# Kernel tuning notes

Measured on AMD Instinct MI355X. Metric: run time of the kernel, lower is better.

Reference implementation:

```python
import jax, jax.numpy as jnp
import numpy as np

N, E, D, H, DH = 10000, 160000, 1024, 4, 256  # nodes, edges, feat dim, heads, per-head dim
NB, G = 3, 64  # num_blocks, num graphs in batch
NEG_SLOPE = 0.2  # PyG GATConv default


def setup_inputs() -> dict:
    key = jax.random.key(0)
    ks = jax.random.split(key, 8)
    x = jax.random.normal(ks[0], (N, D), jnp.float32)
    edge_index = jax.random.randint(ks[1], (2, E), 0, N)
    batch = jnp.sort(jax.random.randint(ks[2], (N,), 0, G))
    W = jax.random.normal(ks[3], (NB, D, H * DH), jnp.float32) * 0.03
    a_src = jax.random.normal(ks[4], (NB, H, DH), jnp.float32) * 0.1
    a_dst = jax.random.normal(ks[5], (NB, H, DH), jnp.float32) * 0.1
    b = jnp.zeros((NB, H * DH), jnp.float32)
    Wr = jax.random.normal(ks[6], (D, 2), jnp.float32) * 0.03
    br = jnp.zeros((2,), jnp.float32)
    return dict(x=x, edge_index=edge_index, batch=batch, W=W, a_src=a_src,
                a_dst=a_dst, b=b, Wr=Wr, br=br)


def _gat_conv(x, src, dst, W, asrc, adst, bias):
    # Linear projection per head: [N, H, DH]
    h = (x @ W).reshape(N, H, DH)
    # Per-node attention logits (src/dst halves of the GAT attention vector)
    es = jnp.einsum('nhd,hd->nh', h, asrc)  # [N, H]
    ed = jnp.einsum('nhd,hd->nh', h, adst)  # [N, H]
    # Edge scores + LeakyReLU
    e = jax.nn.leaky_relu(es[src] + ed[dst], NEG_SLOPE)  # [Etot, H]
    # Segment softmax over edges sharing the same destination node
    m = jax.ops.segment_max(e, dst, num_segments=N)
    p = jnp.exp(e - m[dst])
    s = jax.ops.segment_sum(p, dst, num_segments=N)
    alpha = p / (s[dst] + 1e-16)  # [Etot, H]
    # Scatter-aggregate weighted source features
    out = jax.ops.segment_sum(h[src] * alpha[:, :, None], dst, num_segments=N)
    return out.reshape(N, H * DH) + bias


def reference(x, edge_index, batch, W, a_src, a_dst, b, Wr, br):
    # PyG GATConv adds self-loops by default
    loops = jnp.arange(N)
    src = jnp.concatenate([edge_index[0], loops])
    dst = jnp.concatenate([edge_index[1], loops])
    # Faithful to the source: each block reads the ORIGINAL x; dropout in eval mode.
    h = x
    for i in range(NB):
        h = jax.nn.relu(_gat_conv(x, src, dst, W[i], a_src[i], a_dst[i], b[i]))
    # global_mean_pool over graph assignment `batch`
    sums = jax.ops.segment_sum(h, batch, num_segments=G)
    cnt = jax.ops.segment_sum(jnp.ones((N, 1), h.dtype), batch, num_segments=G)
    pooled = sums / jnp.maximum(cnt, 1.0)
    return pooled @ Wr + br
```

## Files before the change

kernel.cpp:

```cpp
#include <hip/hip_runtime.h>
#include <hip/hip_bf16.h>

#define N_NODES 10000
#define N_EDGES 160000
#define ETOT    (N_NODES + N_EDGES)
#define DIM     1024
#define NHEAD   4
#define DHEAD   256
#define NGRAPH  64
#define NEG_SLOPE 0.2f

typedef short  bf16x8 __attribute__((ext_vector_type(8)));
typedef float  f32x4  __attribute__((ext_vector_type(4)));
typedef unsigned short u16x4 __attribute__((ext_vector_type(4)));
typedef unsigned short u16x8 __attribute__((ext_vector_type(8)));

__device__ __forceinline__ unsigned short f2bf_rne(float v) {
    unsigned u = __builtin_bit_cast(unsigned, v);
    return (unsigned short)((u + 0x7fffu + ((u >> 16) & 1u)) >> 16);
}
__device__ __forceinline__ float bf2f(unsigned short b) {
    return __builtin_bit_cast(float, (unsigned)b << 16);
}
__device__ __forceinline__ float lrelu(float x) { return x > 0.f ? x : NEG_SLOPE * x; }


__global__ __launch_bounds__(256) void prep_x(const float* __restrict__ x,
                                              unsigned short* __restrict__ xhi,
                                              unsigned short* __restrict__ xlo) {
    int i = blockIdx.x * 256 + threadIdx.x;
    if (i >= N_NODES * 128) return;
    int row = i >> 7, kseg = i & 127;
    const float* src = x + (size_t)row * DIM + kseg * 8;
    f32x4 v0 = *(const f32x4*)src;
    f32x4 v1 = *(const f32x4*)(src + 4);
    u16x8 hi, lo;
#pragma unroll
    for (int j = 0; j < 4; ++j) {
        unsigned short hb = f2bf_rne(v0[j]);
        hi[j] = hb; lo[j] = f2bf_rne(v0[j] - bf2f(hb));
    }
#pragma unroll
    for (int j = 0; j < 4; ++j) {
        unsigned short hb = f2bf_rne(v1[j]);
        hi[4 + j] = hb; lo[4 + j] = f2bf_rne(v1[j] - bf2f(hb));
    }
    size_t off = (size_t)(row >> 4) * 16384 + (kseg >> 2) * 512 + (kseg & 3) * 128 + (row & 15) * 8;
    *(u16x8*)(xhi + off) = hi;
    *(u16x8*)(xlo + off) = lo;
}

__global__ __launch_bounds__(256) void prep_w(const float* __restrict__ W2,
                                              unsigned short* __restrict__ wthi,
                                              unsigned short* __restrict__ wtlo,
                                              float* __restrict__ es,
                                              float* __restrict__ ed,
                                              int* __restrict__ cnt,
                                              int* __restrict__ curs,
                                              int* __restrict__ gcnt,
                                              int* __restrict__ gbeg,
                                              int* __restrict__ gend) {
    __shared__ float tile[64][65];
    int bc = blockIdx.x;
    int bk = blockIdx.y;
    int t = threadIdx.x;

    int gid = (blockIdx.y * gridDim.x + blockIdx.x) * 256 + t;
    if (gid < NGRAPH) { gcnt[gid] = 0; gbeg[gid] = 0x7fffffff; gend[gid] = -1; }
    if (gid < N_NODES) { cnt[gid] = 1; curs[gid] = 0; }
    if (gid < N_NODES * 4) { es[gid] = 0.f; ed[gid] = 0.f; }

    int tj = t & 63, ti = t >> 6;
#pragma unroll
    for (int u = 0; u < 16; ++u) {
        int r = u * 4 + ti;
        tile[r][tj] = W2[(size_t)(bk * 64 + r) * DIM + bc * 64 + tj];
    }
    __syncthreads();
#pragma unroll
    for (int u = 0; u < 16; ++u) {
        int cr = u * 4 + ti;
        float v = tile[tj][cr];
        unsigned short hb = f2bf_rne(v);
        float rres = v - bf2f(hb);
        int col = bc * 64 + cr;
        int k = bk * 64 + tj;
        size_t o = (size_t)(col >> 4) * 16384 + (k >> 5) * 512
                 + ((k >> 3) & 3) * 128 + (col & 15) * 8 + (k & 7);
        wthi[o] = hb;
        wtlo[o] = f2bf_rne(rres);
    }
}

#define BM 128
#define BN 128
#define BK 32
#define NROWT ((N_NODES + BM - 1) / BM)
#define NCOLT (DIM / BN)

__global__ __launch_bounds__(256) void gemm3(const unsigned short* __restrict__ xhi,
                                             const unsigned short* __restrict__ xlo,
                                             const unsigned short* __restrict__ wthi,
                                             const unsigned short* __restrict__ wtlo,
                                             const float* __restrict__ asrc,
                                             const float* __restrict__ adst,
                                             unsigned short* __restrict__ hb,
                                             float* __restrict__ es,
                                             float* __restrict__ ed) {
    const int id = blockIdx.x;
    const int xcd = id & 7;
    const int br = xcd + 8 * (id >> 6);
    const int bc = (id >> 3) & 7;
    if (br >= NROWT) return;
    const int r0 = br * BM;
    const int c0 = bc * BN;

    __shared__ short lds[4][BM * BK];
    const int t = threadIdx.x;
    const int lane = t & 63, wid = t >> 6;
    const int wm = wid >> 1, wn = wid & 1;

    const unsigned short* const srcs[4] = {xhi, xlo, wthi, wtlo};
    const int g0 = ((wid < 2) ? r0 : c0) >> 4;
    const unsigned short* gsrc = srcs[wid] + (size_t)g0 * 16384 + (size_t)lane * 8;

    f32x4 acc[4][4];
#pragma unroll
    for (int mi = 0; mi < 4; ++mi)
#pragma unroll
        for (int ni = 0; ni < 4; ++ni) acc[mi][ni] = (f32x4){0.f, 0.f, 0.f, 0.f};

    for (int kt = 0; kt < DIM / BK; ++kt) {
        __syncthreads();
#pragma unroll
        for (int j = 0; j < 8; ++j) {
            const unsigned short* g = gsrc + (size_t)j * 16384 + (size_t)kt * 512;
            __builtin_amdgcn_global_load_lds(
                (const __attribute__((address_space(1))) unsigned int*)g,
                (__attribute__((address_space(3))) unsigned int*)&lds[wid][j * 512],
                16, 0, 0);
        }
        __syncthreads();

        bf16x8 ahi[4], alo[4], bhi[4], blo[4];
#pragma unroll
        for (int mi = 0; mi < 4; ++mi) {
            int sub = wm * 4 + mi;
            ahi[mi] = *(const bf16x8*)&lds[0][sub * 512 + lane * 8];
            alo[mi] = *(const bf16x8*)&lds[1][sub * 512 + lane * 8];
        }
#pragma unroll
        for (int ni = 0; ni < 4; ++ni) {
            int sub = wn * 4 + ni;
            bhi[ni] = *(const bf16x8*)&lds[2][sub * 512 + lane * 8];
            blo[ni] = *(const bf16x8*)&lds[3][sub * 512 + lane * 8];
        }
#pragma unroll
        for (int mi = 0; mi < 4; ++mi)
#pragma unroll
            for (int ni = 0; ni < 4; ++ni) {
                f32x4 c = acc[mi][ni];
                c = __builtin_amdgcn_mfma_f32_16x16x32_bf16(ahi[mi], bhi[ni], c, 0, 0, 0);
                c = __builtin_amdgcn_mfma_f32_16x16x32_bf16(ahi[mi], blo[ni], c, 0, 0, 0);
                c = __builtin_amdgcn_mfma_f32_16x16x32_bf16(alo[mi], bhi[ni], c, 0, 0, 0);
                acc[mi][ni] = c;
            }
    }

#pragma unroll
    for (int mi = 0; mi < 4; ++mi)
#pragma unroll
        for (int ni = 0; ni < 4; ++ni)
#pragma unroll
            for (int v = 0; v < 4; ++v) {
                int row = r0 + wm * 64 + mi * 16 + ((lane >> 4) << 2) + v;
                if (row < N_NODES) {
                    int col = c0 + wn * 64 + ni * 16 + (lane & 15);
                    hb[(size_t)row * DIM + col] = f2bf_rne(acc[mi][ni][v]);
                }
            }

    const int head = c0 >> 8;
    float as_c[4], ad_c[4];
#pragma unroll
    for (int ni = 0; ni < 4; ++ni) {
        int col = c0 + wn * 64 + ni * 16 + (lane & 15);
        as_c[ni] = asrc[col];
        ad_c[ni] = adst[col];
    }
#pragma unroll
    for (int mi = 0; mi < 4; ++mi)
#pragma unroll
        for (int v = 0; v < 4; ++v) {
            float pe = 0.f, pd = 0.f;
#pragma unroll
            for (int ni = 0; ni < 4; ++ni) {
                float a = acc[mi][ni][v];
                pe += a * as_c[ni];
                pd += a * ad_c[ni];
            }
#pragma unroll
            for (int d = 1; d < 16; d <<= 1) {
                pe += __shfl_xor(pe, d);
                pd += __shfl_xor(pd, d);
            }
            int row = r0 + wm * 64 + mi * 16 + ((lane >> 4) << 2) + v;
            if ((lane & 15) == 0 && row < N_NODES) {
                atomicAdd(es + row * 4 + head, pe);
                atomicAdd(ed + row * 4 + head, pd);
            }
        }
}

__global__ void graph_k(const int* __restrict__ dst, const int* __restrict__ batch,
                        int* cnt, int* gcnt, int* gbeg, int* gend) {
    int e = blockIdx.x * 256 + threadIdx.x;
    if (e < N_EDGES) atomicAdd(cnt + dst[e], 1);
    if (e < N_NODES) {
        int b = batch[e];
        atomicAdd(gcnt + b, 1);
        atomicMin(gbeg + b, e);
        atomicMax(gend + b, e);
    }
}

__global__ __launch_bounds__(1024) void scan_k(const int* __restrict__ cnt, int* __restrict__ off) {
    __shared__ int wsh[16];
    __shared__ int tot_s;
    int t = threadIdx.x, lane = t & 63, wv = t >> 6;
    int running = 0;
    for (int c0 = 0; c0 < N_NODES; c0 += 1024) {
        int i = c0 + t;
        int v = (i < N_NODES) ? cnt[i] : 0;
        int s = v;
#pragma unroll
        for (int d = 1; d < 64; d <<= 1) {
            int y = __shfl_up(s, d);
            if (lane >= d) s += y;
        }
        if (lane == 63) wsh[wv] = s;
        __syncthreads();
        if (wv == 0) {
            int wsv = (lane < 16) ? wsh[lane] : 0;
            int e = wsv;
#pragma unroll
            for (int d = 1; d < 16; d <<= 1) {
                int y = __shfl_up(e, d);
                if (lane >= d) e += y;
            }
            if (lane < 16) wsh[lane] = e - wsv;
            if (lane == 15) tot_s = e;
        }
        __syncthreads();
        if (i < N_NODES) off[i] = running + wsh[wv] + s - v;
        running += tot_s;
    }
}

__global__ void bucket_k(const int* __restrict__ src, const int* __restrict__ dst,
                         const int* __restrict__ off, int* cursor, int* bucket) {
    int e = blockIdx.x * 256 + threadIdx.x;
    if (e >= ETOT) return;
    int d = (e < N_EDGES) ? dst[e] : (e - N_EDGES);
    int pos = atomicAdd(cursor + d, 1);
    bucket[off[d] + pos] = e;
}

#define HCAP 192
__global__ __launch_bounds__(256) void aggregate_k(const unsigned short* __restrict__ hb,
                                                   const float* __restrict__ es,
                                                   const float* __restrict__ ed,
                                                   const int* __restrict__ src,
                                                   const int* __restrict__ cnt,
                                                   const int* __restrict__ off,
                                                   const int* __restrict__ bucket,
                                                   const float* __restrict__ b2,
                                                   float* __restrict__ out) {
    int n = blockIdx.x, t = threadIdx.x;
    int deg = cnt[n], base = off[n];
    f32x4 edn = *(const f32x4*)(ed + (size_t)n * 4);
    __shared__ int  s_src[HCAP];
    __shared__ f32x4 s_e[HCAP];
    __shared__ f32x4 wred[4];

    f32x4 m4 = {-3e38f, -3e38f, -3e38f, -3e38f};
    for (int i = t; i < deg; i += 256) {
        int eid = bucket[base + i];
        int s = (eid < N_EDGES) ? src[eid] : (eid - N_EDGES);
        f32x4 e4 = *(const f32x4*)(es + (size_t)s * 4);
        e4.x = lrelu(e4.x + edn.x); e4.y = lrelu(e4.y + edn.y);
        e4.z = lrelu(e4.z + edn.z); e4.w = lrelu(e4.w + edn.w);
        if (i < HCAP) { s_src[i] = s; s_e[i] = e4; }
        m4.x = fmaxf(m4.x, e4.x); m4.y = fmaxf(m4.y, e4.y);
        m4.z = fmaxf(m4.z, e4.z); m4.w = fmaxf(m4.w, e4.w);
    }
#pragma unroll
    for (int d = 1; d < 64; d <<= 1) {
        m4.x = fmaxf(m4.x, __shfl_xor(m4.x, d));
        m4.y = fmaxf(m4.y, __shfl_xor(m4.y, d));
        m4.z = fmaxf(m4.z, __shfl_xor(m4.z, d));
        m4.w = fmaxf(m4.w, __shfl_xor(m4.w, d));
    }
    if ((t & 63) == 0) wred[t >> 6] = m4;
    __syncthreads();
    f32x4 mm = wred[0];
#pragma unroll
    for (int w = 1; w < 4; ++w) {
        mm.x = fmaxf(mm.x, wred[w].x); mm.y = fmaxf(mm.y, wred[w].y);
        mm.z = fmaxf(mm.z, wred[w].z); mm.w = fmaxf(mm.w, wred[w].w);
    }
    int hd = t >> 6;
    float mh = hd == 0 ? mm.x : hd == 1 ? mm.y : hd == 2 ? mm.z : mm.w;

    f32x4 acc = {0.f, 0.f, 0.f, 0.f};
    float sump = 0.f;
    for (int i = 0; i < deg; ++i) {
        int s;
        f32x4 e4;
        if (i < HCAP) { s = s_src[i]; e4 = s_e[i]; }
        else {
            int eid = bucket[base + i];
            s = (eid < N_EDGES) ? src[eid] : (eid - N_EDGES);
            e4 = *(const f32x4*)(es + (size_t)s * 4);
            e4.x = lrelu(e4.x + edn.x); e4.y = lrelu(e4.y + edn.y);
            e4.z = lrelu(e4.z + edn.z); e4.w = lrelu(e4.w + edn.w);
        }
        float eh = hd == 0 ? e4.x : hd == 1 ? e4.y : hd == 2 ? e4.z : e4.w;
        float p = expf(eh - mh);
        sump += p;
        u16x4 q = *(const u16x4*)(hb + (size_t)s * DIM + t * 4);
        f32x4 hv = {bf2f(q[0]), bf2f(q[1]), bf2f(q[2]), bf2f(q[3])};
        acc += p * hv;
    }
    float inv = 1.0f / (sump + 1e-16f);
    f32x4 bb = *(const f32x4*)(b2 + t * 4);
    f32x4 r = acc * inv + bb;
    r.x = fmaxf(r.x, 0.f); r.y = fmaxf(r.y, 0.f);
    r.z = fmaxf(r.z, 0.f); r.w = fmaxf(r.w, 0.f);
    *(f32x4*)(out + (size_t)n * DIM + t * 4) = r;
}

__global__ __launch_bounds__(256) void pool_k(const float* __restrict__ out,
                                              const int* __restrict__ gbeg,
                                              const int* __restrict__ gend,
                                              float* __restrict__ pooled) {
    int g = blockIdx.x, c = blockIdx.y, t = threadIdx.x;
    int col = c * 256 + t;
    int b0 = gbeg[g], b1 = gend[g];
    float acc = 0.f;
    for (int n = b0; n <= b1; ++n) acc += out[(size_t)n * DIM + col];
    pooled[(size_t)g * DIM + col] = acc;
}

__global__ __launch_bounds__(256) void final_k(const float* __restrict__ pooled,
                                               const int* __restrict__ gcnt,
                                               const float* __restrict__ Wr,
                                               const float* __restrict__ br,
                                               float* __restrict__ out) {
    int g = blockIdx.x, t = threadIdx.x;
    float s0 = 0.f, s1 = 0.f;
    for (int d = t; d < DIM; d += 256) {
        float v = pooled[(size_t)g * DIM + d];
        s0 += v * Wr[d * 2];
        s1 += v * Wr[d * 2 + 1];
    }
    __shared__ float r0[256], r1[256];
    r0[t] = s0; r1[t] = s1;
    __syncthreads();
    for (int st = 128; st > 0; st >>= 1) {
        if (t < st) { r0[t] += r0[t + st]; r1[t] += r1[t + st]; }
        __syncthreads();
    }
    if (t == 0) {
        float c = fmaxf((float)gcnt[g], 1.f);
        out[g * 2 + 0] = r0[0] / c + br[0];
        out[g * 2 + 1] = r1[0] / c + br[1];
    }
}

extern "C" void kernel_launch(void* const* d_in, const int* in_sizes, int n_in,
                              void* d_out, int out_size, void* d_ws, size_t ws_size,
                              hipStream_t stream) {
    (void)in_sizes; (void)n_in; (void)out_size; (void)ws_size;
    const float* x     = (const float*)d_in[0];
    const int*   ei    = (const int*)d_in[1];
    const int*   batch = (const int*)d_in[2];
    const float* W     = (const float*)d_in[3];
    const float* a_src = (const float*)d_in[4];
    const float* a_dst = (const float*)d_in[5];
    const float* b     = (const float*)d_in[6];
    const float* Wr    = (const float*)d_in[7];
    const float* br    = (const float*)d_in[8];

    const float* W2    = W + (size_t)2 * DIM * DIM;
    const float* asrc2 = a_src + 2 * NHEAD * DHEAD;
    const float* adst2 = a_dst + 2 * NHEAD * DHEAD;
    const float* b2    = b + 2 * DIM;
    const int* srcI = ei;
    const int* dstI = ei + N_EDGES;

    char* wsp = (char*)d_ws;
    size_t o = 0;
    auto alloc = [&](size_t bytes) -> char* {
        char* p = wsp + o;
        o = (o + bytes + 255) & ~(size_t)255;
        return p;
    };
    unsigned short* xhi  = (unsigned short*)alloc((size_t)N_NODES * DIM * 2);
    unsigned short* xlo  = (unsigned short*)alloc((size_t)N_NODES * DIM * 2);
    unsigned short* wthi = (unsigned short*)alloc((size_t)DIM * DIM * 2);
    unsigned short* wtlo = (unsigned short*)alloc((size_t)DIM * DIM * 2);
    unsigned short* hb   = (unsigned short*)alloc((size_t)N_NODES * DIM * 2);
    float* es   = (float*)alloc((size_t)N_NODES * 4 * 4);
    float* ed   = (float*)alloc((size_t)N_NODES * 4 * 4);
    int*   cnt  = (int*)alloc((size_t)N_NODES * 4);
    int*   offs = (int*)alloc((size_t)N_NODES * 4);
    int*   curs = (int*)alloc((size_t)N_NODES * 4);
    int*   bkt  = (int*)alloc((size_t)ETOT * 4);
    float* pooled = (float*)alloc((size_t)NGRAPH * DIM * 4);
    int*   gcnt   = (int*)alloc(NGRAPH * 4);
    int*   gbeg   = (int*)alloc(NGRAPH * 4);
    int*   gend   = (int*)alloc(NGRAPH * 4);
    float* outn = (float*)xhi;

    prep_x<<<(N_NODES * 128 + 255) / 256, 256, 0, stream>>>(x, xhi, xlo);
    prep_w<<<dim3(16, 16), 256, 0, stream>>>(W2, wthi, wtlo, es, ed, cnt, curs, gcnt, gbeg, gend);
    gemm3<<<((NROWT + 7) / 8) * 8 * NCOLT, 256, 0, stream>>>(xhi, xlo, wthi, wtlo,
                                                             asrc2, adst2, hb, es, ed);
    graph_k<<<(N_EDGES + 255) / 256, 256, 0, stream>>>(dstI, batch, cnt, gcnt, gbeg, gend);
    scan_k<<<1, 1024, 0, stream>>>(cnt, offs);
    bucket_k<<<(ETOT + 255) / 256, 256, 0, stream>>>(srcI, dstI, offs, curs, bkt);

    aggregate_k<<<N_NODES, 256, 0, stream>>>(hb, es, ed, srcI, cnt, offs, bkt, b2, outn);
    pool_k<<<dim3(NGRAPH, 4), 256, 0, stream>>>(outn, gbeg, gend, pooled);
    final_k<<<NGRAPH, 256, 0, stream>>>(pooled, gcnt, Wr, br, (float*)d_out);
}
```

Baseline: 422.8 us.

## Use row-major bf16 split layout, fuse prep with graph stats and pooling

Drops the pre-tiled 16-row MFMA layout for x and W. Both are now stored row-major as bf16 hi/lo, and the GEMM loads them with strided global_load_lds over a plain 2D grid, without the XCD-aware block swizzle. The x split conversion is merged with the edge/graph counting kernel into one launch, and mean-pooling is fused with the final linear head. The goal is fewer launches and no pooled buffer, at the cost of less coalesced global loads, possible LDS bank conflicts in the GEMM, and a pooling stage with fewer blocks.

```diff
diff --git a/kernel.cpp b/kernel.cpp
--- a/kernel.cpp
+++ b/kernel.cpp
@@ -24,31 +24,6 @@
 }
 __device__ __forceinline__ float lrelu(float x) { return x > 0.f ? x : NEG_SLOPE * x; }
 
-
-__global__ __launch_bounds__(256) void prep_x(const float* __restrict__ x,
-                                              unsigned short* __restrict__ xhi,
-                                              unsigned short* __restrict__ xlo) {
-    int i = blockIdx.x * 256 + threadIdx.x;
-    if (i >= N_NODES * 128) return;
-    int row = i >> 7, kseg = i & 127;
-    const float* src = x + (size_t)row * DIM + kseg * 8;
-    f32x4 v0 = *(const f32x4*)src;
-    f32x4 v1 = *(const f32x4*)(src + 4);
-    u16x8 hi, lo;
-#pragma unroll
-    for (int j = 0; j < 4; ++j) {
-        unsigned short hb = f2bf_rne(v0[j]);
-        hi[j] = hb; lo[j] = f2bf_rne(v0[j] - bf2f(hb));
-    }
-#pragma unroll
-    for (int j = 0; j < 4; ++j) {
-        unsigned short hb = f2bf_rne(v1[j]);
-        hi[4 + j] = hb; lo[4 + j] = f2bf_rne(v1[j] - bf2f(hb));
-    }
-    size_t off = (size_t)(row >> 4) * 16384 + (kseg >> 2) * 512 + (kseg & 3) * 128 + (row & 15) * 8;
-    *(u16x8*)(xhi + off) = hi;
-    *(u16x8*)(xlo + off) = lo;
-}
 
 __global__ __launch_bounds__(256) void prep_w(const float* __restrict__ W2,
                                               unsigned short* __restrict__ wthi,
@@ -83,12 +58,45 @@
         float v = tile[tj][cr];
         unsigned short hb = f2bf_rne(v);
         float rres = v - bf2f(hb);
-        int col = bc * 64 + cr;
-        int k = bk * 64 + tj;
-        size_t o = (size_t)(col >> 4) * 16384 + (k >> 5) * 512
-                 + ((k >> 3) & 3) * 128 + (col & 15) * 8 + (k & 7);
+        size_t o = (size_t)(bc * 64 + cr) * DIM + bk * 64 + tj;
         wthi[o] = hb;
         wtlo[o] = f2bf_rne(rres);
+    }
+}
+
+#define XBLK (N_NODES * DIM / 4 / 256)
+__global__ __launch_bounds__(256) void prep_xg(const float* __restrict__ x,
+                                               unsigned short* __restrict__ xhi,
+                                               unsigned short* __restrict__ xlo,
+                                               const int* __restrict__ dst,
+                                               const int* __restrict__ batch,
+                                               int* __restrict__ cnt,
+                                               int* __restrict__ gcnt,
+                                               int* __restrict__ gbeg,
+                                               int* __restrict__ gend) {
+    int bid = blockIdx.x;
+    if (bid < XBLK) {
+        int i = bid * 256 + threadIdx.x;
+        f32x4 v = *(const f32x4*)(x + (size_t)i * 4);
+        u16x4 hi, lo;
+#pragma unroll
+        for (int j = 0; j < 4; ++j) {
+            unsigned short hb = f2bf_rne(v[j]);
+            float r = v[j] - bf2f(hb);
+            hi[j] = hb;
+            lo[j] = f2bf_rne(r);
+        }
+        *(u16x4*)(xhi + (size_t)i * 4) = hi;
+        *(u16x4*)(xlo + (size_t)i * 4) = lo;
+    } else {
+        int e = (bid - XBLK) * 256 + threadIdx.x;
+        if (e < N_EDGES) atomicAdd(cnt + dst[e], 1);
+        if (e < N_NODES) {
+            int b = batch[e];
+            atomicAdd(gcnt + b, 1);
+            atomicMin(gbeg + b, e);
+            atomicMax(gend + b, e);
+        }
     }
 }
 
@@ -107,13 +115,8 @@
                                              unsigned short* __restrict__ hb,
                                              float* __restrict__ es,
                                              float* __restrict__ ed) {
-    const int id = blockIdx.x;
-    const int xcd = id & 7;
-    const int br = xcd + 8 * (id >> 6);
-    const int bc = (id >> 3) & 7;
-    if (br >= NROWT) return;
-    const int r0 = br * BM;
-    const int c0 = bc * BN;
+    const int r0 = blockIdx.y * BM;
+    const int c0 = blockIdx.x * BN;
 
     __shared__ short lds[4][BM * BK];
     const int t = threadIdx.x;
@@ -121,8 +124,8 @@
     const int wm = wid >> 1, wn = wid & 1;
 
     const unsigned short* const srcs[4] = {xhi, xlo, wthi, wtlo};
-    const int g0 = ((wid < 2) ? r0 : c0) >> 4;
-    const unsigned short* gsrc = srcs[wid] + (size_t)g0 * 16384 + (size_t)lane * 8;
+    const unsigned short* wbase = srcs[wid];
+    const int rowb = (wid < 2) ? r0 : c0;
 
     f32x4 acc[4][4];
 #pragma unroll
@@ -130,11 +133,15 @@
 #pragma unroll
         for (int ni = 0; ni < 4; ++ni) acc[mi][ni] = (f32x4){0.f, 0.f, 0.f, 0.f};
 
-    for (int kt = 0; kt < DIM / BK; ++kt) {
+    const int rL = lane & 15;
+    const int koff = (lane >> 4) * 8;
+
+    for (int k0 = 0; k0 < DIM; k0 += BK) {
         __syncthreads();
 #pragma unroll
         for (int j = 0; j < 8; ++j) {
-            const unsigned short* g = gsrc + (size_t)j * 16384 + (size_t)kt * 512;
+            const unsigned short* g = wbase
+                + (size_t)(rowb + j * 16 + (lane >> 2)) * DIM + k0 + (lane & 3) * 8;
             __builtin_amdgcn_global_load_lds(
                 (const __attribute__((address_space(1))) unsigned int*)g,
                 (__attribute__((address_space(3))) unsigned int*)&lds[wid][j * 512],
@@ -145,15 +152,15 @@
         bf16x8 ahi[4], alo[4], bhi[4], blo[4];
 #pragma unroll
         for (int mi = 0; mi < 4; ++mi) {
-            int sub = wm * 4 + mi;
-            ahi[mi] = *(const bf16x8*)&lds[0][sub * 512 + lane * 8];
-            alo[mi] = *(const bf16x8*)&lds[1][sub * 512 + lane * 8];
+            int row = wm * 64 + mi * 16 + rL;
+            ahi[mi] = *(const bf16x8*)&lds[0][row * BK + koff];
+            alo[mi] = *(const bf16x8*)&lds[1][row * BK + koff];
         }
 #pragma unroll
         for (int ni = 0; ni < 4; ++ni) {
-            int sub = wn * 4 + ni;
-            bhi[ni] = *(const bf16x8*)&lds[2][sub * 512 + lane * 8];
-            blo[ni] = *(const bf16x8*)&lds[3][sub * 512 + lane * 8];
+            int row = wn * 64 + ni * 16 + rL;
+            bhi[ni] = *(const bf16x8*)&lds[2][row * BK + koff];
+            blo[ni] = *(const bf16x8*)&lds[3][row * BK + koff];
         }
 #pragma unroll
         for (int mi = 0; mi < 4; ++mi)
@@ -210,18 +217,6 @@
                 atomicAdd(ed + row * 4 + head, pd);
             }
         }
-}
-
-__global__ void graph_k(const int* __restrict__ dst, const int* __restrict__ batch,
-                        int* cnt, int* gcnt, int* gbeg, int* gend) {
-    int e = blockIdx.x * 256 + threadIdx.x;
-    if (e < N_EDGES) atomicAdd(cnt + dst[e], 1);
-    if (e < N_NODES) {
-        int b = batch[e];
-        atomicAdd(gcnt + b, 1);
-        atomicMin(gbeg + b, e);
-        atomicMax(gend + b, e);
-    }
 }
 
 __global__ __launch_bounds__(1024) void scan_k(const int* __restrict__ cnt, int* __restrict__ off) {
@@ -340,41 +335,34 @@
     *(f32x4*)(out + (size_t)n * DIM + t * 4) = r;
 }
 
-__global__ __launch_bounds__(256) void pool_k(const float* __restrict__ out,
-                                              const int* __restrict__ gbeg,
-                                              const int* __restrict__ gend,
-                                              float* __restrict__ pooled) {
-    int g = blockIdx.x, c = blockIdx.y, t = threadIdx.x;
-    int col = c * 256 + t;
+__global__ __launch_bounds__(256) void poolfinal_k(const float* __restrict__ outn,
+                                                   const int* __restrict__ gcnt,
+                                                   const int* __restrict__ gbeg,
+                                                   const int* __restrict__ gend,
+                                                   const float* __restrict__ Wr,
+                                                   const float* __restrict__ br,
+                                                   float* __restrict__ out) {
+    int g = blockIdx.x, t = threadIdx.x;
     int b0 = gbeg[g], b1 = gend[g];
-    float acc = 0.f;
-    for (int n = b0; n <= b1; ++n) acc += out[(size_t)n * DIM + col];
-    pooled[(size_t)g * DIM + col] = acc;
-}
-
-__global__ __launch_bounds__(256) void final_k(const float* __restrict__ pooled,
-                                               const int* __restrict__ gcnt,
-                                               const float* __restrict__ Wr,
-                                               const float* __restrict__ br,
-                                               float* __restrict__ out) {
-    int g = blockIdx.x, t = threadIdx.x;
-    float s0 = 0.f, s1 = 0.f;
-    for (int d = t; d < DIM; d += 256) {
-        float v = pooled[(size_t)g * DIM + d];
-        s0 += v * Wr[d * 2];
-        s1 += v * Wr[d * 2 + 1];
-    }
-    __shared__ float r0[256], r1[256];
-    r0[t] = s0; r1[t] = s1;
+    f32x4 acc = {0.f, 0.f, 0.f, 0.f};
+    for (int n = b0; n <= b1; ++n)
+        acc += *(const f32x4*)(outn + (size_t)n * DIM + t * 4);
+    int c4 = t * 4;
+    float s0 = acc.x * Wr[c4 * 2]     + acc.y * Wr[(c4 + 1) * 2]
+             + acc.z * Wr[(c4 + 2) * 2] + acc.w * Wr[(c4 + 3) * 2];
+    float s1 = acc.x * Wr[c4 * 2 + 1]     + acc.y * Wr[(c4 + 1) * 2 + 1]
+             + acc.z * Wr[(c4 + 2) * 2 + 1] + acc.w * Wr[(c4 + 3) * 2 + 1];
+    __shared__ float r0s[256], r1s[256];
+    r0s[t] = s0; r1s[t] = s1;
     __syncthreads();
     for (int st = 128; st > 0; st >>= 1) {
-        if (t < st) { r0[t] += r0[t + st]; r1[t] += r1[t + st]; }
+        if (t < st) { r0s[t] += r0s[t + st]; r1s[t] += r1s[t + st]; }
         __syncthreads();
     }
     if (t == 0) {
         float c = fmaxf((float)gcnt[g], 1.f);
-        out[g * 2 + 0] = r0[0] / c + br[0];
-        out[g * 2 + 1] = r1[0] / c + br[1];
+        out[g * 2 + 0] = r0s[0] / c + br[0];
+        out[g * 2 + 1] = r1s[0] / c + br[1];
     }
 }
 
@@ -417,21 +405,20 @@
     int*   offs = (int*)alloc((size_t)N_NODES * 4);
     int*   curs = (int*)alloc((size_t)N_NODES * 4);
     int*   bkt  = (int*)alloc((size_t)ETOT * 4);
-    float* pooled = (float*)alloc((size_t)NGRAPH * DIM * 4);
     int*   gcnt   = (int*)alloc(NGRAPH * 4);
     int*   gbeg   = (int*)alloc(NGRAPH * 4);
     int*   gend   = (int*)alloc(NGRAPH * 4);
     float* outn = (float*)xhi;
 
-    prep_x<<<(N_NODES * 128 + 255) / 256, 256, 0, stream>>>(x, xhi, xlo);
-    prep_w<<<dim3(16, 16), 256, 0, stream>>>(W2, wthi, wtlo, es, ed, cnt, curs, gcnt, gbeg, gend);
-    gemm3<<<((NROWT + 7) / 8) * 8 * NCOLT, 256, 0, stream>>>(xhi, xlo, wthi, wtlo,
-                                                             asrc2, adst2, hb, es, ed);
-    graph_k<<<(N_EDGES + 255) / 256, 256, 0, stream>>>(dstI, batch, cnt, gcnt, gbeg, gend);
+    prep_w<<<dim3(16, 16), 256, 0, stream>>>(W2, wthi, wtlo, es, ed, cnt, curs,
+                                             gcnt, gbeg, gend);
+    prep_xg<<<XBLK + (N_EDGES + 255) / 256, 256, 0, stream>>>(x, xhi, xlo, dstI, batch,
+                                                              cnt, gcnt, gbeg, gend);
+    gemm3<<<dim3(NCOLT, NROWT), 256, 0, stream>>>(xhi, xlo, wthi, wtlo,
+                                                  asrc2, adst2, hb, es, ed);
     scan_k<<<1, 1024, 0, stream>>>(cnt, offs);
     bucket_k<<<(ETOT + 255) / 256, 256, 0, stream>>>(srcI, dstI, offs, curs, bkt);
 
     aggregate_k<<<N_NODES, 256, 0, stream>>>(hb, es, ed, srcI, cnt, offs, bkt, b2, outn);
-    pool_k<<<dim3(NGRAPH, 4), 256, 0, stream>>>(outn, gbeg, gend, pooled);
-    final_k<<<NGRAPH, 256, 0, stream>>>(pooled, gcnt, Wr, br, (float*)d_out);
-}
+    poolfinal_k<<<NGRAPH, 256, 0, stream>>>(outn, gcnt, gbeg, gend, Wr, br, (float*)d_out);
+}
```

New measurement: 408.3 us. -3.4%, faster.
